# Performance work log

Hardware: AMD Instinct MI355X
Metric: run time of the kernel (lower is better)

The kernel has to match this reference:

```python
import jax, jax.numpy as jnp
import numpy as np

BOUND = 10.0
EPS = 1e-06
MIN_SCALE = 1e-4


def _params_to_spline(raw_w, raw_h, raw_s, bound):
    # Standard Durkan et al. rational-quadratic spline parameterization.
    # raw_w/raw_h: (1, D, K); raw_s: (1, D, K+1)
    two_b = 2.0 * bound
    widths = jax.nn.softmax(raw_w[0], axis=-1) * two_b      # (D, K)
    heights = jax.nn.softmax(raw_h[0], axis=-1) * two_b     # (D, K)
    zero = jnp.zeros(widths.shape[:-1] + (1,), widths.dtype)
    xk = -bound + jnp.concatenate([zero, jnp.cumsum(widths, axis=-1)], axis=-1)   # (D, K+1)
    yk = -bound + jnp.concatenate([zero, jnp.cumsum(heights, axis=-1)], axis=-1)  # (D, K+1)
    slopes = jax.nn.softplus(raw_s[0])                       # (D, K+1)
    return xk, yk, widths, heights, slopes


def _rqs_forward(z, xk, yk, widths, heights, slopes, bound):
    # z: (B, D); per-dim knots xk/yk: (D, K+1); widths/heights: (D, K); slopes: (D, K+1)
    B, D = z.shape
    K = widths.shape[-1]
    zc = jnp.clip(z, -bound, bound)
    # per-dim binary search over knot positions
    idx = jax.vmap(lambda knots, col: jnp.searchsorted(knots, col, side='right'),
                   in_axes=(0, 1), out_axes=1)(xk, zc) - 1
    idx = jnp.clip(idx, 0, K - 1)                            # (B, D)
    di = jnp.arange(D)[None, :]
    xk_sel = xk[di, idx]
    w_sel = widths[di, idx]
    yk_sel = yk[di, idx]
    h_sel = heights[di, idx]
    d0 = slopes[di, idx]
    d1 = slopes[di, idx + 1]
    theta = (zc - xk_sel) / w_sel
    s = h_sel / w_sel
    t1m = theta * (1.0 - theta)
    den = s + (d0 + d1 - 2.0 * s) * t1m
    y_in = yk_sel + h_sel * (s * theta * theta + d0 * t1m) / den
    inside = (z > -bound) & (z < bound)
    return jnp.where(inside, y_in, z)


def setup_inputs() -> dict:
    key = jax.random.key(0)
    ks = jax.random.split(key, 7)
    B, D, K = 8192, 1024, 64
    return {
        'u': jax.random.uniform(ks[0], (B, D), dtype=jnp.float32),
        'tau': jax.random.normal(ks[1], (B, 1), dtype=jnp.float32),
        'log_scale': jax.random.normal(ks[2], (D,), dtype=jnp.float32) * 0.1,
        'bias': jax.random.normal(ks[3], (D,), dtype=jnp.float32) * 0.1,
        'raw_w': jax.random.normal(ks[4], (1, D, K), dtype=jnp.float32) * 0.5,
        'raw_h': jax.random.normal(ks[5], (1, D, K), dtype=jnp.float32) * 0.5,
        'raw_s': jax.random.normal(ks[6], (1, D, K + 1), dtype=jnp.float32) * 0.5,
    }


def reference(u, tau, log_scale, bias, raw_w, raw_h, raw_s):
    # logit input transform
    u_safe = jnp.clip(u, EPS, 1.0 - EPS)
    z = jnp.log(u_safe) - jnp.log1p(-u_safe)
    xk, yk, widths, heights, slopes = _params_to_spline(raw_w, raw_h, raw_s, BOUND)
    z = _rqs_forward(z, xk, yk, widths, heights, slopes, BOUND)
    scale = jax.nn.softplus(log_scale) + MIN_SCALE
    q = z * scale[None, :] + bias[None, :]
    return tau * q  # tau (B,1) broadcasts to (B,D)
```

## Files before the change

### kernel.cpp

```cpp
#include <hip/hip_runtime.h>
#include <math.h>

#define BOUNDF 10.0f
#define EPSF 1e-6f
#define MIN_SCALEF 1e-4f
#define DD 1024
#define KK 64
#define KP1 65

#define TD 32
#define TR 64

typedef float vf4 __attribute__((ext_vector_type(4)));

__global__ __launch_bounds__(64) void rqs_precompute(
    const float* __restrict__ raw_w, const float* __restrict__ raw_h,
    const float* __restrict__ raw_s, const float* __restrict__ log_scale,
    float* __restrict__ xk, float* __restrict__ yk,
    float* __restrict__ sl, float* __restrict__ scale)
{
    const int d = blockIdx.x;
    const int k = threadIdx.x;

    float ew = __expf(raw_w[d * KK + k]);
    float eh = __expf(raw_h[d * KK + k]);

    float sw = ew, sh = eh;
#pragma unroll
    for (int off = 1; off < 64; off <<= 1) {
        sw += __shfl_xor(sw, off, 64);
        sh += __shfl_xor(sh, off, 64);
    }
    float wk = ew * (2.0f * BOUNDF) / sw;
    float hk = eh * (2.0f * BOUNDF) / sh;

    float cw = wk, ch = hk;
#pragma unroll
    for (int off = 1; off < 64; off <<= 1) {
        float tw = __shfl_up(cw, off, 64);
        float th = __shfl_up(ch, off, 64);
        if (k >= off) { cw += tw; ch += th; }
    }
    xk[d * KP1 + k + 1] = -BOUNDF + cw;
    yk[d * KP1 + k + 1] = -BOUNDF + ch;

    float rs = raw_s[d * KP1 + k];
    sl[d * KP1 + k] = log1pf(__expf(rs));
    if (k == 0) {
        xk[d * KP1] = -BOUNDF;
        yk[d * KP1] = -BOUNDF;
        float rs2 = raw_s[d * KP1 + KK];
        sl[d * KP1 + KK] = log1pf(__expf(rs2));
        scale[d] = log1pf(__expf(log_scale[d])) + MIN_SCALEF;
    }
}

__global__ __launch_bounds__(256, 6) void rqs_main(
    const float* __restrict__ u, const float* __restrict__ tau,
    const float* __restrict__ bias,
    const float* __restrict__ xk_g, const float* __restrict__ yk_g,
    const float* __restrict__ sl_g, const float* __restrict__ scale_g,
    float* __restrict__ out)
{
    __shared__ float lxk[TD * KP1];
    __shared__ float lyk[TD * KP1];
    __shared__ float lsl[TD * KP1];

    const int bx = blockIdx.x;
    const int dchunk = bx & (DD / TD - 1);
    const int rchunk = bx >> 5;
    const int d0 = dchunk * TD;
    const int r0 = rchunk * TR;
    const int t = threadIdx.x;

    for (int i = t; i < TD * KP1; i += 256) {
        lxk[i] = xk_g[d0 * KP1 + i];
        lyk[i] = yk_g[d0 * KP1 + i];
        lsl[i] = sl_g[d0 * KP1 + i];
    }
    __syncthreads();

    const int g = t & 7;
    const int rlane = t >> 3;
    const int dl = g * 4;
    const int dg = d0 + dl;

    float sc[4], bi[4];
    float kreg[4][7];
#pragma unroll
    for (int j = 0; j < 4; ++j) {
        sc[j] = scale_g[dg + j];
        bi[j] = bias[dg + j];
        const int base = (dl + j) * KP1;
#pragma unroll
        for (int i = 0; i < 7; ++i) kreg[j][i] = lxk[base + 8 * (i + 1)];
    }

    int b = r0 + rlane;
    vf4 uu = __builtin_nontemporal_load((const vf4*)(u + (size_t)b * DD + dg));
    float tb = tau[b];

#pragma unroll 1
    for (int it = 0; it < TR / 32; ++it) {
        const int bcur = b;
        const vf4 ucur = uu;
        const float tcur = tb;
        if (it + 1 < TR / 32) {
            const int bn = bcur + 32;
            uu = __builtin_nontemporal_load((const vf4*)(u + (size_t)bn * DD + dg));
            tb = tau[bn];
            b = bn;
        }
        float ua[4] = {ucur.x, ucur.y, ucur.z, ucur.w};
        float res[4];
#pragma unroll
        for (int j = 0; j < 4; ++j) {
            float uv = fminf(fmaxf(ua[j], EPSF), 1.0f - EPSF);
            float z = __logf(uv * __builtin_amdgcn_rcpf(1.0f - uv));
            float zc = fminf(fmaxf(z, -BOUNDF), BOUNDF);
            const int base = (dl + j) * KP1;
            int lo = (zc >= kreg[j][3]) ? 32 : 0;
            float m16 = (lo & 32) ? kreg[j][5] : kreg[j][1];
            lo += (zc >= m16) ? 16 : 0;
            float a8 = (lo & 32) ? kreg[j][4] : kreg[j][0];
            float b8 = (lo & 32) ? kreg[j][6] : kreg[j][2];
            float m8 = (lo & 16) ? b8 : a8;
            lo += (zc >= m8) ? 8 : 0;
            lo += (lxk[base + lo + 4] <= zc) ? 4 : 0;
            lo += (lxk[base + lo + 2] <= zc) ? 2 : 0;
            lo += (lxk[base + lo + 1] <= zc) ? 1 : 0;
            float x0 = lxk[base + lo], x1 = lxk[base + lo + 1];
            float y0 = lyk[base + lo], y1 = lyk[base + lo + 1];
            float s0 = lsl[base + lo], s1 = lsl[base + lo + 1];
            float w = x1 - x0, h = y1 - y0;
            float invw = __builtin_amdgcn_rcpf(w);
            float th = (zc - x0) * invw;
            float sm = h * invw;
            float t1m = th * (1.0f - th);
            float den = fmaf(fmaf(-2.0f, sm, s0 + s1), t1m, sm);
            float num = h * fmaf(sm * th, th, s0 * t1m);
            float y = fmaf(num, __builtin_amdgcn_rcpf(den), y0);
            y = (z > -BOUNDF && z < BOUNDF) ? y : z;
            res[j] = tcur * fmaf(y, sc[j], bi[j]);
        }
        vf4 ro;
        ro.x = res[0];
        ro.y = res[1];
        ro.z = res[2];
        ro.w = res[3];
        __builtin_nontemporal_store(ro, (vf4*)(out + (size_t)bcur * DD + dg));
    }
}

extern "C" void kernel_launch(void* const* d_in, const int* in_sizes, int n_in,
                              void* d_out, int out_size, void* d_ws, size_t ws_size,
                              hipStream_t stream)
{
    const float* u         = (const float*)d_in[0];
    const float* tau       = (const float*)d_in[1];
    const float* log_scale = (const float*)d_in[2];
    const float* bias      = (const float*)d_in[3];
    const float* raw_w     = (const float*)d_in[4];
    const float* raw_h     = (const float*)d_in[5];
    const float* raw_s     = (const float*)d_in[6];
    float* out = (float*)d_out;

    float* ws    = (float*)d_ws;
    float* xk    = ws;
    float* yk    = xk + DD * KP1;
    float* sl    = yk + DD * KP1;
    float* scale = sl + DD * KP1;

    const int B = in_sizes[0] / DD;

    rqs_precompute<<<DD, 64, 0, stream>>>(raw_w, raw_h, raw_s, log_scale,
                                          xk, yk, sl, scale);
    rqs_main<<<(DD / TD) * (B / TR), 256, 0, stream>>>(u, tau, bias,
                                                       xk, yk, sl, scale, out);
}
```

Measured before the change: 116.5 us.

## Fuse spline precompute into main kernel and recompute knots per block

```diff
diff --git a/kernel.cpp b/kernel.cpp
--- a/kernel.cpp
+++ b/kernel.cpp
@@ -9,57 +9,15 @@
 #define KP1 65
 
 #define TD 32
-#define TR 64
+#define TR 128
 
 typedef float vf4 __attribute__((ext_vector_type(4)));
 
-__global__ __launch_bounds__(64) void rqs_precompute(
+__global__ __launch_bounds__(256, 6) void rqs_fused(
+    const float* __restrict__ u, const float* __restrict__ tau,
+    const float* __restrict__ log_scale, const float* __restrict__ bias,
     const float* __restrict__ raw_w, const float* __restrict__ raw_h,
-    const float* __restrict__ raw_s, const float* __restrict__ log_scale,
-    float* __restrict__ xk, float* __restrict__ yk,
-    float* __restrict__ sl, float* __restrict__ scale)
-{
-    const int d = blockIdx.x;
-    const int k = threadIdx.x;
-
-    float ew = __expf(raw_w[d * KK + k]);
-    float eh = __expf(raw_h[d * KK + k]);
-
-    float sw = ew, sh = eh;
-#pragma unroll
-    for (int off = 1; off < 64; off <<= 1) {
-        sw += __shfl_xor(sw, off, 64);
-        sh += __shfl_xor(sh, off, 64);
-    }
-    float wk = ew * (2.0f * BOUNDF) / sw;
-    float hk = eh * (2.0f * BOUNDF) / sh;
-
-    float cw = wk, ch = hk;
-#pragma unroll
-    for (int off = 1; off < 64; off <<= 1) {
-        float tw = __shfl_up(cw, off, 64);
-        float th = __shfl_up(ch, off, 64);
-        if (k >= off) { cw += tw; ch += th; }
-    }
-    xk[d * KP1 + k + 1] = -BOUNDF + cw;
-    yk[d * KP1 + k + 1] = -BOUNDF + ch;
-
-    float rs = raw_s[d * KP1 + k];
-    sl[d * KP1 + k] = log1pf(__expf(rs));
-    if (k == 0) {
-        xk[d * KP1] = -BOUNDF;
-        yk[d * KP1] = -BOUNDF;
-        float rs2 = raw_s[d * KP1 + KK];
-        sl[d * KP1 + KK] = log1pf(__expf(rs2));
-        scale[d] = log1pf(__expf(log_scale[d])) + MIN_SCALEF;
-    }
-}
-
-__global__ __launch_bounds__(256, 6) void rqs_main(
-    const float* __restrict__ u, const float* __restrict__ tau,
-    const float* __restrict__ bias,
-    const float* __restrict__ xk_g, const float* __restrict__ yk_g,
-    const float* __restrict__ sl_g, const float* __restrict__ scale_g,
+    const float* __restrict__ raw_s,
     float* __restrict__ out)
 {
     __shared__ float lxk[TD * KP1];
@@ -73,10 +31,41 @@
     const int r0 = rchunk * TR;
     const int t = threadIdx.x;
 
-    for (int i = t; i < TD * KP1; i += 256) {
-        lxk[i] = xk_g[d0 * KP1 + i];
-        lyk[i] = yk_g[d0 * KP1 + i];
-        lsl[i] = sl_g[d0 * KP1 + i];
+    {
+        const int wave = t >> 6;
+        const int lane = t & 63;
+#pragma unroll 1
+        for (int jj = 0; jj < 8; ++jj) {
+            const int ld = wave * 8 + jj;
+            const int d = d0 + ld;
+            float ew = __expf(raw_w[d * KK + lane]);
+            float eh = __expf(raw_h[d * KK + lane]);
+            float sw = ew, sh = eh;
+#pragma unroll
+            for (int off = 1; off < 64; off <<= 1) {
+                sw += __shfl_xor(sw, off, 64);
+                sh += __shfl_xor(sh, off, 64);
+            }
+            float wk = ew * (2.0f * BOUNDF) * __builtin_amdgcn_rcpf(sw);
+            float hk = eh * (2.0f * BOUNDF) * __builtin_amdgcn_rcpf(sh);
+            float cw = wk, ch = hk;
+#pragma unroll
+            for (int off = 1; off < 64; off <<= 1) {
+                float tw = __shfl_up(cw, off, 64);
+                float th = __shfl_up(ch, off, 64);
+                if (lane >= off) { cw += tw; ch += th; }
+            }
+            lxk[ld * KP1 + lane + 1] = -BOUNDF + cw;
+            lyk[ld * KP1 + lane + 1] = -BOUNDF + ch;
+            float rs = raw_s[d * KP1 + lane];
+            lsl[ld * KP1 + lane] = log1pf(__expf(rs));
+            if (lane == 0) {
+                lxk[ld * KP1] = -BOUNDF;
+                lyk[ld * KP1] = -BOUNDF;
+                float rs2 = raw_s[d * KP1 + KK];
+                lsl[ld * KP1 + KK] = log1pf(__expf(rs2));
+            }
+        }
     }
     __syncthreads();
 
@@ -89,7 +78,7 @@
     float kreg[4][7];
 #pragma unroll
     for (int j = 0; j < 4; ++j) {
-        sc[j] = scale_g[dg + j];
+        sc[j] = log1pf(__expf(log_scale[dg + j])) + MIN_SCALEF;
         bi[j] = bias[dg + j];
         const int base = (dl + j) * KP1;
 #pragma unroll
@@ -97,7 +86,7 @@
     }
 
     int b = r0 + rlane;
-    vf4 uu = __builtin_nontemporal_load((const vf4*)(u + (size_t)b * DD + dg));
+    vf4 uu = *(const vf4*)(u + (size_t)b * DD + dg);
     float tb = tau[b];
 
 #pragma unroll 1
@@ -107,7 +96,7 @@
         const float tcur = tb;
         if (it + 1 < TR / 32) {
             const int bn = bcur + 32;
-            uu = __builtin_nontemporal_load((const vf4*)(u + (size_t)bn * DD + dg));
+            uu = *(const vf4*)(u + (size_t)bn * DD + dg);
             tb = tau[bn];
             b = bn;
         }
@@ -119,17 +108,47 @@
             float z = __logf(uv * __builtin_amdgcn_rcpf(1.0f - uv));
             float zc = fminf(fmaxf(z, -BOUNDF), BOUNDF);
             const int base = (dl + j) * KP1;
-            int lo = (zc >= kreg[j][3]) ? 32 : 0;
-            float m16 = (lo & 32) ? kreg[j][5] : kreg[j][1];
-            lo += (zc >= m16) ? 16 : 0;
-            float a8 = (lo & 32) ? kreg[j][4] : kreg[j][0];
-            float b8 = (lo & 32) ? kreg[j][6] : kreg[j][2];
-            float m8 = (lo & 16) ? b8 : a8;
-            lo += (zc >= m8) ? 8 : 0;
-            lo += (lxk[base + lo + 4] <= zc) ? 4 : 0;
-            lo += (lxk[base + lo + 2] <= zc) ? 2 : 0;
-            lo += (lxk[base + lo + 1] <= zc) ? 1 : 0;
-            float x0 = lxk[base + lo], x1 = lxk[base + lo + 1];
+            float xlo = -BOUNDF, xhi = BOUNDF;
+            int lo;
+            {
+                float m = kreg[j][3];
+                bool c = (zc >= m);
+                lo = c ? 32 : 0;
+                xlo = c ? m : xlo;  xhi = c ? xhi : m;
+            }
+            {
+                float m = (lo & 32) ? kreg[j][5] : kreg[j][1];
+                bool c = (zc >= m);
+                lo += c ? 16 : 0;
+                xlo = c ? m : xlo;  xhi = c ? xhi : m;
+            }
+            {
+                float a8 = (lo & 32) ? kreg[j][4] : kreg[j][0];
+                float b8 = (lo & 32) ? kreg[j][6] : kreg[j][2];
+                float m = (lo & 16) ? b8 : a8;
+                bool c = (zc >= m);
+                lo += c ? 8 : 0;
+                xlo = c ? m : xlo;  xhi = c ? xhi : m;
+            }
+            {
+                float m = lxk[base + lo + 4];
+                bool c = (m <= zc);
+                lo += c ? 4 : 0;
+                xlo = c ? m : xlo;  xhi = c ? xhi : m;
+            }
+            {
+                float m = lxk[base + lo + 2];
+                bool c = (m <= zc);
+                lo += c ? 2 : 0;
+                xlo = c ? m : xlo;  xhi = c ? xhi : m;
+            }
+            {
+                float m = lxk[base + lo + 1];
+                bool c = (m <= zc);
+                lo += c ? 1 : 0;
+                xlo = c ? m : xlo;  xhi = c ? xhi : m;
+            }
+            float x0 = xlo, x1 = xhi;
             float y0 = lyk[base + lo], y1 = lyk[base + lo + 1];
             float s0 = lsl[base + lo], s1 = lsl[base + lo + 1];
             float w = x1 - x0, h = y1 - y0;
@@ -148,7 +167,7 @@
         ro.y = res[1];
         ro.z = res[2];
         ro.w = res[3];
-        __builtin_nontemporal_store(ro, (vf4*)(out + (size_t)bcur * DD + dg));
+        *(vf4*)(out + (size_t)bcur * DD + dg) = ro;
     }
 }
 
@@ -165,16 +184,8 @@
     const float* raw_s     = (const float*)d_in[6];
     float* out = (float*)d_out;
 
-    float* ws    = (float*)d_ws;
-    float* xk    = ws;
-    float* yk    = xk + DD * KP1;
-    float* sl    = yk + DD * KP1;
-    float* scale = sl + DD * KP1;
-
     const int B = in_sizes[0] / DD;
 
-    rqs_precompute<<<DD, 64, 0, stream>>>(raw_w, raw_h, raw_s, log_scale,
-                                          xk, yk, sl, scale);
-    rqs_main<<<(DD / TD) * (B / TR), 256, 0, stream>>>(u, tau, bias,
-                                                       xk, yk, sl, scale, out);
+    rqs_fused<<<(DD / TD) * (B / TR), 256, 0, stream>>>(
+        u, tau, log_scale, bias, raw_w, raw_h, raw_s, out);
 }
```

New measurement: 134.8 us. 1.16x slower.
